# Kernel optimization log

Hardware: AMD Instinct MI355X
Metric: run time of the kernel (lower is better)

Reference implementation:

```python
import jax, jax.numpy as jnp
import numpy as np

IN_C, OUT_C, K, STRIDE, PAD = 128, 256, 3, 1, 1

def setup_inputs() -> dict:
    key = jax.random.key(0)
    kx, kw = jax.random.split(key)
    x = jax.random.normal(kx, (32, IN_C, 56, 56), dtype=jnp.float32)
    # xavier_uniform_ on W: bound = sqrt(6 / (fan_in + fan_out)), fan = C*K*K
    fan_in = IN_C * K * K
    fan_out = OUT_C * K * K
    bound = float(np.sqrt(6.0 / (fan_in + fan_out)))
    W = jax.random.uniform(kw, (OUT_C, IN_C, K, K), dtype=jnp.float32, minval=-bound, maxval=bound)
    b = jnp.zeros((OUT_C,), dtype=jnp.float32)
    return {"x": x, "W": W, "b": b}

def reference(x, W, b):
    # Direct conv: NCHW input, OIHW weights -> NCHW output
    out = jax.lax.conv_general_dilated(
        x, W,
        window_strides=(STRIDE, STRIDE),
        padding=[(PAD, PAD), (PAD, PAD)],
        dimension_numbers=("NCHW", "OIHW", "NCHW"),
    )
    return out + b[None, :, None, None]
```

## Files before the change

kernel.cpp:

```cpp
#include <hip/hip_runtime.h>


typedef unsigned short u16;
typedef _Float16 f16x8 __attribute__((ext_vector_type(8)));
typedef float f32x4 __attribute__((ext_vector_type(4)));

#define CIN    128
#define COUT   256
#define HW     56
#define NPIX   3136
#define TOTPIX 100352
#define NKT    18

#define WAITVM0 asm volatile("s_waitcnt vmcnt(0)" ::: "memory")
#define BARRIER asm volatile("s_barrier" ::: "memory")

__device__ __forceinline__ void gload16(const void* g, void* l) {
  __builtin_amdgcn_global_load_lds(
      (const __attribute__((address_space(1))) void*)g,
      (__attribute__((address_space(3))) void*)l, 16, 0, 0);
}

__device__ __forceinline__ u16 f2h(float f) {
  _Float16 h = (_Float16)f;
  return __builtin_bit_cast(u16, h);
}

__global__ void prep_w(const float* __restrict__ W, u16* __restrict__ Wt,
                       u16* __restrict__ zp) {
  int e = blockIdx.x * 256 + threadIdx.x;
  if (blockIdx.x == 0 && threadIdx.x < 128) zp[threadIdx.x] = 0;
  int j   = e & 7;
  int ocl = (e >> 3) & 127;
  int k8  = (e >> 10) & 7;
  int o   = (e >> 13) & 1;
  int t   = e >> 14;
  int oc = o * 128 + ocl;
  int ic = (t & 1) * 64 + k8 * 8 + j;
  Wt[e] = f2h(W[(oc * CIN + ic) * 9 + (t >> 1)]);
}

__global__ void prep_x(const float* __restrict__ x, u16* __restrict__ xt) {
  int b = blockIdx.x;
  int n = b >> 6, g = (b >> 2) & 15, c = b & 3;
  const float* xs = x + ((size_t)(n * 16 + g) * 8) * NPIX;
  u16* xd = xt + ((size_t)(n * 16 + g) * NPIX) * 8;
  #pragma unroll
  for (int i = 0; i < 4; ++i) {
    int off = i * 256 + (int)threadIdx.x;
    if (off < 784) {
      int pix = c * 784 + off;
      unsigned q0, q1, q2, q3;
      q0 = (unsigned)f2h(xs[(size_t)0 * NPIX + pix]) |
           ((unsigned)f2h(xs[(size_t)1 * NPIX + pix]) << 16);
      q1 = (unsigned)f2h(xs[(size_t)2 * NPIX + pix]) |
           ((unsigned)f2h(xs[(size_t)3 * NPIX + pix]) << 16);
      q2 = (unsigned)f2h(xs[(size_t)4 * NPIX + pix]) |
           ((unsigned)f2h(xs[(size_t)5 * NPIX + pix]) << 16);
      q3 = (unsigned)f2h(xs[(size_t)6 * NPIX + pix]) |
           ((unsigned)f2h(xs[(size_t)7 * NPIX + pix]) << 16);
      uint4 v; v.x = q0; v.y = q1; v.z = q2; v.w = q3;
      *(uint4*)(xd + (size_t)pix * 8) = v;
    }
  }
}

__global__ __launch_bounds__(256, 4) void conv_mfma(
    const u16* __restrict__ Wt, const u16* __restrict__ xt,
    const float* __restrict__ bias, float* __restrict__ out,
    const u16* __restrict__ zp) {
  __shared__ __align__(16) u16 lds[16384];

  int tid  = threadIdx.x;
  int lane = tid & 63;
  int wv   = tid >> 6;
  int bid  = blockIdx.x;
  int wgid = (bid & 7) * 196 + (bid >> 3);
  int octile = wgid & 1;
  int ptile  = wgid >> 1;

  int wm = wv >> 1, wn = wv & 1;
  int l15 = lane & 15, lg = lane >> 4;

  int spix = tid & 127;
  int p = ptile * 128 + spix;
  int sn = p / NPIX, sr = p % NPIX, sy = sr / HW, sx = sr % HW;
  const char* xtb = (const char*)xt;
  const char* zpc = (const char*)zp;
  const char* wbase = (const char*)Wt + (size_t)octile * 16384 + tid * 16;

  auto stage = [&](int t) {
    const char* asrc = wbase + (size_t)t * 32768;
    #pragma unroll
    for (int i = 0; i < 4; ++i)
      gload16(asrc + i * 4096, &lds[tid * 8 + i * 2048]);
    int tap = t >> 1, ich = t & 1;
    int t3 = tap / 3;
    int dh = t3 - 1, dw = (tap - t3 * 3) - 1;
    bool ok = (unsigned)(sy + dh) < HW && (unsigned)(sx + dw) < HW;
    const char* bsrc = ok
        ? xtb + ((size_t)(sn * 16 + ich * 8 + (tid >> 7)) * NPIX +
                 (sr + dh * HW + dw)) * 16
        : zpc;
    size_t step = ok ? (size_t)2 * NPIX * 16 : 0;
    u16* bdst = &lds[8192 + ((tid >> 7) * 128 + spix) * 8];
    #pragma unroll
    for (int i = 0; i < 4; ++i)
      gload16(bsrc + i * step, bdst + i * 2048);
  };

  f32x4 acc[4][4] = {};

  stage(0);
  WAITVM0; BARRIER;

  for (int t = 0; t < NKT; ++t) {
    #pragma unroll
    for (int kk = 0; kk < 2; ++kk) {
      f16x8 af[4], bf[4];
      #pragma unroll
      for (int q = 0; q < 4; ++q)
        af[q] = *(const f16x8*)
            &lds[((kk * 4 + lg) * 128 + wm * 64 + q * 16 + l15) * 8];
      #pragma unroll
      for (int q = 0; q < 4; ++q)
        bf[q] = *(const f16x8*)
            &lds[8192 + ((kk * 4 + lg) * 128 + wn * 64 + q * 16 + l15) * 8];
      __builtin_amdgcn_s_setprio(1);
      #pragma unroll
      for (int mq = 0; mq < 4; ++mq)
        #pragma unroll
        for (int nf = 0; nf < 4; ++nf)
          acc[mq][nf] = __builtin_amdgcn_mfma_f32_16x16x32_f16(
              af[mq], bf[nf], acc[mq][nf], 0, 0, 0);
      __builtin_amdgcn_s_setprio(0);
    }
    if (t + 1 < NKT) {
      BARRIER;
      stage(t + 1);
      WAITVM0; BARRIER;
    }
  }

  float* ob[4];
  #pragma unroll
  for (int nf = 0; nf < 4; ++nf) {
    int pp = ptile * 128 + wn * 64 + nf * 16 + l15;
    int nn = pp / NPIX, hw = pp % NPIX;
    ob[nf] = out + (size_t)nn * COUT * NPIX + hw;
  }
  #pragma unroll
  for (int mq = 0; mq < 4; ++mq) {
    int oc = octile * 128 + wm * 64 + mq * 16 + lg * 4;
    f32x4 bv = *(const f32x4*)&bias[oc];
    #pragma unroll
    for (int rr = 0; rr < 4; ++rr) {
      size_t row = (size_t)(oc + rr) * NPIX;
      #pragma unroll
      for (int nf = 0; nf < 4; ++nf)
        ob[nf][row] = acc[mq][nf][rr] + bv[rr];
    }
  }
}

__global__ void conv_naive(const float* __restrict__ x, const float* __restrict__ W,
                           const float* __restrict__ b, float* __restrict__ out) {
  int idx = blockIdx.x * 256 + threadIdx.x;
  int hw = idx % NPIX;
  int tmp = idx / NPIX;
  int oc = tmp % COUT;
  int n = tmp / COUT;
  int h = hw / HW, w = hw % HW;
  float acc = b[oc];
  for (int ic = 0; ic < CIN; ++ic) {
    const float* xr = x + (size_t)(n * CIN + ic) * NPIX;
    const float* wr = W + (size_t)(oc * CIN + ic) * 9;
    #pragma unroll
    for (int kh = 0; kh < 3; ++kh) {
      int ih = h + kh - 1;
      if ((unsigned)ih >= HW) continue;
      #pragma unroll
      for (int kw = 0; kw < 3; ++kw) {
        int iw = w + kw - 1;
        if ((unsigned)iw >= HW) continue;
        acc += xr[ih * HW + iw] * wr[kh * 3 + kw];
      }
    }
  }
  out[idx] = acc;
}

extern "C" void kernel_launch(void* const* d_in, const int* in_sizes, int n_in,
                              void* d_out, int out_size, void* d_ws, size_t ws_size,
                              hipStream_t stream) {
  const float* x = (const float*)d_in[0];
  const float* W = (const float*)d_in[1];
  const float* b = (const float*)d_in[2];
  float* out = (float*)d_out;

  const size_t ZP_OFF = 0;
  const size_t WT_OFF = 256;
  const size_t XT_OFF = 256 + 589824;
  const size_t NEED = XT_OFF + (size_t)TOTPIX * CIN * 2;

  if (ws_size < NEED) {
    conv_naive<<<TOTPIX * COUT / 256, 256, 0, stream>>>(x, W, b, out);
    return;
  }
  char* ws = (char*)d_ws;
  u16* zp = (u16*)(ws + ZP_OFF);
  u16* Wt = (u16*)(ws + WT_OFF);
  u16* xt = (u16*)(ws + XT_OFF);

  prep_w<<<1152, 256, 0, stream>>>(W, Wt, zp);
  prep_x<<<2048, 256, 0, stream>>>(x, xt);
  conv_mfma<<<1568, 256, 0, stream>>>(Wt, xt, b, out, zp);
}
```

Before: 90.53 us.

## Double-buffer weight tiles in LDS and load activations directly into registers

Activation (B) fragments are now read straight from global memory into registers, using precomputed per-lane offsets and a padding validity bitmask, instead of being staged through LDS. Weight tiles are double-buffered in LDS and the loop is unrolled by two so the loads for step t+1 are issued before the MFMAs of step t. This aims to hide global-load latency and remove half of the LDS traffic and one barrier per step. In exchange it uses more registers (occupancy bound lowered from 4 to 3) and issues uncoalesced 16-byte global reads for activations, since each lane reads a strided location.

```diff
diff --git a/kernel.cpp b/kernel.cpp
--- a/kernel.cpp
+++ b/kernel.cpp
@@ -65,7 +65,7 @@
   }
 }
 
-__global__ __launch_bounds__(256, 4) void conv_mfma(
+__global__ __launch_bounds__(256, 3) void conv_mfma(
     const u16* __restrict__ Wt, const u16* __restrict__ xt,
     const float* __restrict__ bias, float* __restrict__ out,
     const u16* __restrict__ zp) {
@@ -82,64 +82,86 @@
   int wm = wv >> 1, wn = wv & 1;
   int l15 = lane & 15, lg = lane >> 4;
 
-  int spix = tid & 127;
-  int p = ptile * 128 + spix;
-  int sn = p / NPIX, sr = p % NPIX, sy = sr / HW, sx = sr % HW;
-  const char* xtb = (const char*)xt;
-  const char* zpc = (const char*)zp;
+  const char* xtb  = (const char*)xt;
+  const char* zpc  = (const char*)zp;
   const char* wbase = (const char*)Wt + (size_t)octile * 16384 + tid * 16;
 
-  auto stage = [&](int t) {
-    const char* asrc = wbase + (size_t)t * 32768;
+  unsigned boff[4];
+  unsigned long long vmask = 0ull;
+  #pragma unroll
+  for (int nf = 0; nf < 4; ++nf) {
+    int p = ptile * 128 + wn * 64 + nf * 16 + l15;
+    int n = p / NPIX, r = p % NPIX, y = r / HW, x = r % HW;
+    boff[nf] = (unsigned)(((n * 16 + lg) * NPIX + r) * 16);
+    #pragma unroll
+    for (int tap = 0; tap < 9; ++tap) {
+      int dh = tap / 3 - 1, dw = tap % 3 - 1;
+      unsigned long long ok =
+          ((unsigned)(y + dh) < HW && (unsigned)(x + dw) < HW) ? 1ull : 0ull;
+      vmask |= ok << (nf * 9 + tap);
+    }
+  }
+
+  auto stageA = [&](int t) {
+    const char* src = wbase + (size_t)t * 32768;
+    u16* dst = &lds[(t & 1) * 8192 + tid * 8];
     #pragma unroll
     for (int i = 0; i < 4; ++i)
-      gload16(asrc + i * 4096, &lds[tid * 8 + i * 2048]);
+      gload16(src + i * 4096, dst + i * 2048);
+  };
+
+  auto loadB = [&](int t, f16x8 (&bf)[2][4]) {
     int tap = t >> 1, ich = t & 1;
     int t3 = tap / 3;
     int dh = t3 - 1, dw = (tap - t3 * 3) - 1;
-    bool ok = (unsigned)(sy + dh) < HW && (unsigned)(sx + dw) < HW;
-    const char* bsrc = ok
-        ? xtb + ((size_t)(sn * 16 + ich * 8 + (tid >> 7)) * NPIX +
-                 (sr + dh * HW + dw)) * 16
-        : zpc;
-    size_t step = ok ? (size_t)2 * NPIX * 16 : 0;
-    u16* bdst = &lds[8192 + ((tid >> 7) * 128 + spix) * 8];
-    #pragma unroll
-    for (int i = 0; i < 4; ++i)
-      gload16(bsrc + i * step, bdst + i * 2048);
+    int psh = (dh * HW + dw) * 16;
+    #pragma unroll
+    for (int kk = 0; kk < 2; ++kk) {
+      int gsh = (ich * 8 + kk * 4) * NPIX * 16 + psh;
+      #pragma unroll
+      for (int nf = 0; nf < 4; ++nf) {
+        bool ok = (vmask >> (nf * 9 + tap)) & 1ull;
+        const char* sp = ok ? xtb + ((int)boff[nf] + gsh) : zpc;
+        bf[kk][nf] = *(const f16x8*)sp;
+      }
+    }
   };
 
   f32x4 acc[4][4] = {};
 
-  stage(0);
-  WAITVM0; BARRIER;
-
-  for (int t = 0; t < NKT; ++t) {
+  auto compute = [&](int t, const f16x8 (&bf)[2][4]) {
+    const u16* abase = &lds[(t & 1) * 8192];
     #pragma unroll
     for (int kk = 0; kk < 2; ++kk) {
-      f16x8 af[4], bf[4];
+      f16x8 af[4];
       #pragma unroll
       for (int q = 0; q < 4; ++q)
         af[q] = *(const f16x8*)
-            &lds[((kk * 4 + lg) * 128 + wm * 64 + q * 16 + l15) * 8];
-      #pragma unroll
-      for (int q = 0; q < 4; ++q)
-        bf[q] = *(const f16x8*)
-            &lds[8192 + ((kk * 4 + lg) * 128 + wn * 64 + q * 16 + l15) * 8];
+            &abase[((kk * 4 + lg) * 128 + wm * 64 + q * 16 + l15) * 8];
       __builtin_amdgcn_s_setprio(1);
       #pragma unroll
       for (int mq = 0; mq < 4; ++mq)
         #pragma unroll
         for (int nf = 0; nf < 4; ++nf)
           acc[mq][nf] = __builtin_amdgcn_mfma_f32_16x16x32_f16(
-              af[mq], bf[nf], acc[mq][nf], 0, 0, 0);
+              af[mq], bf[kk][nf], acc[mq][nf], 0, 0, 0);
       __builtin_amdgcn_s_setprio(0);
     }
-    if (t + 1 < NKT) {
-      BARRIER;
-      stage(t + 1);
-      WAITVM0; BARRIER;
-    }
+  };
+
+  f16x8 bfA[2][4], bfB[2][4];
+
+  loadB(0, bfA); stageA(0);
+  WAITVM0; BARRIER;
+
+  for (int t = 0; t < NKT; t += 2) {
+    loadB(t + 1, bfB); stageA(t + 1);
+    compute(t, bfA);
+    WAITVM0;
+    BARRIER;
+    if (t + 2 < NKT) { loadB(t + 2, bfA); stageA(t + 2); }
+    compute(t + 1, bfB);
+    if (t + 2 < NKT) { WAITVM0; BARRIER; }
   }
 
   float* ob[4];
```

After: 178.0 us. 1.97x slower.
